# Kernel tuning notes

Measured on AMD Instinct MI355X. Metric: run time of the kernel, lower is better.

The kernel has to match this reference:

```python
import jax, jax.numpy as jnp
import numpy as np

B, S, D, H = 4, 2048, 1024, 16
HD = D // H


def setup_inputs() -> dict:
    key = jax.random.key(0)
    k = jax.random.split(key, 5)
    scale = 0.02
    return {
        "x": jax.random.normal(k[0], (B, S, D), dtype=jnp.float32),
        "Wq": jax.random.normal(k[1], (D, D), dtype=jnp.float32) * scale,
        "Wk": jax.random.normal(k[2], (D, D), dtype=jnp.float32) * scale,
        "Wv": jax.random.normal(k[3], (D, D), dtype=jnp.float32) * scale,
        "Wo": jax.random.normal(k[4], (D, D), dtype=jnp.float32) * scale,
    }


def reference(x, Wq, Wk, Wv, Wo):
    b, s, d_in = x.shape
    h, hd = H, HD
    # projections: [b, s, h, hd] -> [b, h, s, hd]
    q = (x @ Wq).reshape(b, s, h, hd).transpose(0, 2, 1, 3)
    k = (x @ Wk).reshape(b, s, h, hd).transpose(0, 2, 1, 3)
    v = (x @ Wv).reshape(b, s, h, hd).transpose(0, 2, 1, 3)
    # attention scores [b, h, s, s] with causal mask (match original: mask BEFORE scaling)
    scores = jnp.einsum("bhqd,bhkd->bhqk", q, k)
    causal = jnp.triu(jnp.ones((s, s), dtype=bool), k=1)
    scores = jnp.where(causal, -jnp.inf, scores)
    weights = jax.nn.softmax(scores / jnp.sqrt(jnp.float32(hd)), axis=-1)
    ctx = jnp.einsum("bhqk,bhkd->bhqd", weights, v)  # [b, h, s, hd]
    ctx = ctx.transpose(0, 2, 1, 3).reshape(b, s, h * hd)
    return ctx @ Wo
```

## Files before the change

kernel.cpp:

```cpp
#include <hip/hip_runtime.h>

#define SEQ 2048
#define DMODEL 1024
#define NH 16
#define HD 64

typedef unsigned short bf16u;
typedef unsigned short u16x8 __attribute__((ext_vector_type(8)));
typedef unsigned short u16x4 __attribute__((ext_vector_type(4)));
typedef float f32x4 __attribute__((ext_vector_type(4)));

__device__ __forceinline__ unsigned short f2b(float f) {
  __bf16 h = (__bf16)f;
  return __builtin_bit_cast(unsigned short, h);
}

__device__ __forceinline__ f32x4 mfma_bf16(u16x8 a, u16x8 b, f32x4 c) {
  return __builtin_amdgcn_mfma_f32_16x16x32_bf16(a, b, c, 0, 0, 0);
}

__device__ __forceinline__ void load16_lds(const bf16u* g, bf16u* l) {
  __builtin_amdgcn_global_load_lds(
      (const __attribute__((address_space(1))) unsigned int*)(const void*)g,
      (__attribute__((address_space(3))) unsigned int*)(void*)l, 16, 0, 0);
}

__global__ __launch_bounds__(256) void cast_x_kernel(const float4* __restrict__ x,
                                                     u16x4* __restrict__ xb, int n4) {
  int i = blockIdx.x * blockDim.x + threadIdx.x;
  if (i < n4) {
    float4 v = x[i];
    u16x4 o;
    o[0] = f2b(v.x); o[1] = f2b(v.y); o[2] = f2b(v.z); o[3] = f2b(v.w);
    xb[i] = o;
  }
}

__global__ __launch_bounds__(256) void transpose_w_kernel(const float* __restrict__ W0,
                                                          const float* __restrict__ W1,
                                                          const float* __restrict__ W2,
                                                          const float* __restrict__ W3,
                                                          bf16u* __restrict__ T) {
  const float* W = (blockIdx.z == 0) ? W0 : (blockIdx.z == 1) ? W1
                  : (blockIdx.z == 2) ? W2 : W3;
  bf16u* Wt = T + (size_t)blockIdx.z * (DMODEL * DMODEL);
  __shared__ float tile[32][33];
  int n = blockIdx.x * 32 + threadIdx.x;
  int k0 = blockIdx.y * 32;
  for (int i = threadIdx.y; i < 32; i += 8)
    tile[i][threadIdx.x] = W[(size_t)(k0 + i) * DMODEL + n];
  __syncthreads();
  int k = k0 + threadIdx.x;
  int n0 = blockIdx.x * 32;
  for (int i = threadIdx.y; i < 32; i += 8)
    Wt[(size_t)(n0 + i) * DMODEL + k] = f2b(tile[threadIdx.x][i]);
}


__global__ __launch_bounds__(256) void gemm_qkv_kernel(const bf16u* __restrict__ A,
                                                       const bf16u* __restrict__ Wt,
                                                       bf16u* __restrict__ QKV) {
  const bf16u* Bt = Wt + (size_t)blockIdx.z * (DMODEL * DMODEL);
  bf16u* O = QKV + (size_t)blockIdx.z * ((size_t)8192 * DMODEL);
  const bool vmode = (blockIdx.z == 2);

  __shared__ __align__(16) bf16u As[128 * 32];
  __shared__ __align__(16) bf16u Bs[128 * 32];

  const int tid = threadIdx.x;
  const int lane = tid & 63, quad = lane >> 4, l15 = lane & 15;
  const int wave = tid >> 6;
  const int wrow = (wave >> 1) * 64, wcol = (wave & 1) * 64;
  const int mbase = blockIdx.y * 128, nbase = blockIdx.x * 128;

  const int r0 = tid >> 2, s0 = tid & 3;
  const int g0 = s0 ^ (r0 & 3);
  const bf16u* Ag0 = A + (size_t)(mbase + r0) * DMODEL + g0 * 8;
  const bf16u* Bg0 = Bt + (size_t)(nbase + r0) * DMODEL + g0 * 8;
  const bf16u* Ag1 = Ag0 + (size_t)64 * DMODEL;
  const bf16u* Bg1 = Bg0 + (size_t)64 * DMODEL;
  bf16u* Al0 = &As[tid * 8];
  bf16u* Al1 = &As[2048 + tid * 8];
  bf16u* Bl0 = &Bs[tid * 8];
  bf16u* Bl1 = &Bs[2048 + tid * 8];

  const int xq = (quad ^ (l15 & 3)) * 8;

  f32x4 acc[4][4];
#pragma unroll
  for (int i = 0; i < 4; ++i)
#pragma unroll
    for (int j = 0; j < 4; ++j) acc[i][j] = (f32x4){0.f, 0.f, 0.f, 0.f};

  for (int k0 = 0; k0 < DMODEL; k0 += 32) {
    __syncthreads();
    load16_lds(Ag0 + k0, Al0);
    load16_lds(Ag1 + k0, Al1);
    load16_lds(Bg0 + k0, Bl0);
    load16_lds(Bg1 + k0, Bl1);
    __syncthreads();
    u16x8 af[4], bfr[4];
#pragma unroll
    for (int i = 0; i < 4; ++i)
      af[i] = *(const u16x8*)&As[(wrow + i * 16 + l15) * 32 + xq];
#pragma unroll
    for (int j = 0; j < 4; ++j)
      bfr[j] = *(const u16x8*)&Bs[(wcol + j * 16 + l15) * 32 + xq];
#pragma unroll
    for (int i = 0; i < 4; ++i)
#pragma unroll
      for (int j = 0; j < 4; ++j)
        acc[i][j] = mfma_bf16(af[i], bfr[j], acc[i][j]);
  }

#pragma unroll
  for (int i = 0; i < 4; ++i) {
    const int mrow = mbase + wrow + i * 16 + quad * 4;
    const int bb = mrow >> 11, ss = mrow & 2047;
#pragma unroll
    for (int j = 0; j < 4; ++j) {
      const int n = nbase + wcol + j * 16 + l15;
      const int h = n >> 6, hd = n & 63;
      if (vmode) {
        u16x4 pk;
#pragma unroll
        for (int r = 0; r < 4; ++r) pk[r] = f2b(acc[i][j][r]);
        *(u16x4*)&O[(((size_t)(bb * NH + h)) * HD + hd) * SEQ + ss] = pk;
      } else {
#pragma unroll
        for (int r = 0; r < 4; ++r)
          O[(((size_t)(bb * NH + h)) * SEQ + ss + r) * HD + hd] = f2b(acc[i][j][r]);
      }
    }
  }
}

__global__ __launch_bounds__(256) void gemm_out_kernel(const bf16u* __restrict__ A,
                                                       const bf16u* __restrict__ Bt,
                                                       float* __restrict__ Of) {
  __shared__ __align__(16) bf16u As[128 * 32];
  __shared__ __align__(16) bf16u Bs[128 * 32];

  const int tid = threadIdx.x;
  const int lane = tid & 63, quad = lane >> 4, l15 = lane & 15;
  const int wave = tid >> 6;
  const int wrow = (wave >> 1) * 64, wcol = (wave & 1) * 64;
  const int mbase = blockIdx.y * 128, nbase = blockIdx.x * 128;

  const int r0 = tid >> 2, s0 = tid & 3;
  const int g0 = s0 ^ (r0 & 3);
  const bf16u* Ag0 = A + (size_t)(mbase + r0) * DMODEL + g0 * 8;
  const bf16u* Bg0 = Bt + (size_t)(nbase + r0) * DMODEL + g0 * 8;
  const bf16u* Ag1 = Ag0 + (size_t)64 * DMODEL;
  const bf16u* Bg1 = Bg0 + (size_t)64 * DMODEL;
  bf16u* Al0 = &As[tid * 8];
  bf16u* Al1 = &As[2048 + tid * 8];
  bf16u* Bl0 = &Bs[tid * 8];
  bf16u* Bl1 = &Bs[2048 + tid * 8];

  const int xq = (quad ^ (l15 & 3)) * 8;

  f32x4 acc[4][4];
#pragma unroll
  for (int i = 0; i < 4; ++i)
#pragma unroll
    for (int j = 0; j < 4; ++j) acc[i][j] = (f32x4){0.f, 0.f, 0.f, 0.f};

  for (int k0 = 0; k0 < DMODEL; k0 += 32) {
    __syncthreads();
    load16_lds(Ag0 + k0, Al0);
    load16_lds(Ag1 + k0, Al1);
    load16_lds(Bg0 + k0, Bl0);
    load16_lds(Bg1 + k0, Bl1);
    __syncthreads();
    u16x8 af[4], bfr[4];
#pragma unroll
    for (int i = 0; i < 4; ++i)
      af[i] = *(const u16x8*)&As[(wrow + i * 16 + l15) * 32 + xq];
#pragma unroll
    for (int j = 0; j < 4; ++j)
      bfr[j] = *(const u16x8*)&Bs[(wcol + j * 16 + l15) * 32 + xq];
#pragma unroll
    for (int i = 0; i < 4; ++i)
#pragma unroll
      for (int j = 0; j < 4; ++j)
        acc[i][j] = mfma_bf16(af[i], bfr[j], acc[i][j]);
  }

#pragma unroll
  for (int i = 0; i < 4; ++i) {
    const int mrow = mbase + wrow + i * 16 + quad * 4;
#pragma unroll
    for (int j = 0; j < 4; ++j) {
      const int n = nbase + wcol + j * 16 + l15;
#pragma unroll
      for (int r = 0; r < 4; ++r)
        Of[(size_t)(mrow + r) * DMODEL + n] = acc[i][j][r];
    }
  }
}

__global__ __launch_bounds__(256, 2) void attn_kernel(const bf16u* __restrict__ Q,
                                                      const bf16u* __restrict__ K,
                                                      const bf16u* __restrict__ Vt,
                                                      bf16u* __restrict__ ctx) {
  const int bh = blockIdx.y;
  const int b = bh >> 4, h = bh & 15;
  const int bp = blockIdx.x;
  const size_t base = (size_t)bh * SEQ * HD;
  const bf16u* Qb = Q + base;
  const bf16u* Kb = K + base;
  const bf16u* Vb = Vt + base;

  const int tid = threadIdx.x;
  const int wave = tid >> 6, lane = tid & 63, quad = lane >> 4, l15 = lane & 15;

  __shared__ __align__(16) bf16u Ks[64 * 72];
  __shared__ __align__(16) bf16u Vs[64 * 72];
  __shared__ __align__(16) bf16u Ps[4][32 * 68];

  const int srow = tid >> 3;
  const int scol = (tid & 7) * 8;
  const float S = 0.18033688f;

  u16x8 ones;
#pragma unroll
  for (int i = 0; i < 8; ++i) ones[i] = 0x3F80;

#pragma unroll 1
  for (int pi = 0; pi < 2; ++pi) {
    const int qt = pi ? bp : (15 - bp);
    const int qrow0 = qt * 128 + wave * 32;
    const int ntiles = 2 * qt + 2;

    u16x8 aq[2][2];
#pragma unroll
    for (int rt = 0; rt < 2; ++rt)
#pragma unroll
      for (int ch = 0; ch < 2; ++ch)
        aq[rt][ch] = *(const u16x8*)(Qb + (size_t)(qrow0 + rt * 16 + l15) * HD + ch * 32 + quad * 8);

    f32x4 acc[2][4], accl[2];
#pragma unroll
    for (int rt = 0; rt < 2; ++rt) {
#pragma unroll
      for (int nc = 0; nc < 4; ++nc) acc[rt][nc] = (f32x4){0.f, 0.f, 0.f, 0.f};
      accl[rt] = (f32x4){0.f, 0.f, 0.f, 0.f};
    }

    u16x8 kr0 = *(const u16x8*)(Kb + (size_t)srow * HD + scol);
    u16x8 kr1 = *(const u16x8*)(Kb + (size_t)(srow + 32) * HD + scol);
    u16x8 vr0 = *(const u16x8*)(Vb + (size_t)srow * SEQ + scol);
    u16x8 vr1 = *(const u16x8*)(Vb + (size_t)(srow + 32) * SEQ + scol);

#pragma unroll 1
    for (int kt = 0; kt < ntiles; ++kt) {
      const int kbase = kt * 64;
      __syncthreads();
      *(u16x8*)&Ks[srow * 72 + scol] = kr0;
      *(u16x8*)&Ks[(srow + 32) * 72 + scol] = kr1;
      *(u16x8*)&Vs[srow * 72 + scol] = vr0;
      *(u16x8*)&Vs[(srow + 32) * 72 + scol] = vr1;
      __syncthreads();
      if (kt + 1 < ntiles) {
        const int nb = kbase + 64;
        kr0 = *(const u16x8*)(Kb + (size_t)(nb + srow) * HD + scol);
        kr1 = *(const u16x8*)(Kb + (size_t)(nb + srow + 32) * HD + scol);
        vr0 = *(const u16x8*)(Vb + (size_t)srow * SEQ + nb + scol);
        vr1 = *(const u16x8*)(Vb + (size_t)(srow + 32) * SEQ + nb + scol);
      }
      if (kbase > qrow0 + 31) continue;

      f32x4 sc[2][4];
#pragma unroll
      for (int ct = 0; ct < 4; ++ct) {
        u16x8 bk0 = *(const u16x8*)&Ks[(ct * 16 + l15) * 72 + quad * 8];
        u16x8 bk1 = *(const u16x8*)&Ks[(ct * 16 + l15) * 72 + 32 + quad * 8];
#pragma unroll
        for (int rt = 0; rt < 2; ++rt) {
          f32x4 z = {0.f, 0.f, 0.f, 0.f};
          z = mfma_bf16(aq[rt][0], bk0, z);
          z = mfma_bf16(aq[rt][1], bk1, z);
          sc[rt][ct] = z;
        }
      }

      const bool needmask = (kbase + 63 > qrow0);
#pragma unroll
      for (int rt = 0; rt < 2; ++rt) {
#pragma unroll
        for (int r = 0; r < 4; ++r) {
          const int row = qrow0 + rt * 16 + quad * 4 + r;
          float e0 = exp2f(sc[rt][0][r] * S);
          float e1 = exp2f(sc[rt][1][r] * S);
          float e2 = exp2f(sc[rt][2][r] * S);
          float e3 = exp2f(sc[rt][3][r] * S);
          if (needmask) {
            if (kbase + l15 > row) e0 = 0.f;
            if (kbase + 16 + l15 > row) e1 = 0.f;
            if (kbase + 32 + l15 > row) e2 = 0.f;
            if (kbase + 48 + l15 > row) e3 = 0.f;
          }
          const int prow = (rt * 16 + quad * 4 + r) * 68;
          Ps[wave][prow + l15] = f2b(e0);
          Ps[wave][prow + 16 + l15] = f2b(e1);
          Ps[wave][prow + 32 + l15] = f2b(e2);
          Ps[wave][prow + 48 + l15] = f2b(e3);
        }
      }

      u16x8 pa[2][2];
#pragma unroll
      for (int rt = 0; rt < 2; ++rt)
#pragma unroll
        for (int ch = 0; ch < 2; ++ch)
          pa[rt][ch] = *(const u16x8*)&Ps[wave][(rt * 16 + l15) * 68 + ch * 32 + quad * 8];

#pragma unroll
      for (int nc = 0; nc < 4; ++nc) {
        u16x8 bv0 = *(const u16x8*)&Vs[(nc * 16 + l15) * 72 + quad * 8];
        u16x8 bv1 = *(const u16x8*)&Vs[(nc * 16 + l15) * 72 + 32 + quad * 8];
#pragma unroll
        for (int rt = 0; rt < 2; ++rt) {
          acc[rt][nc] = mfma_bf16(pa[rt][0], bv0, acc[rt][nc]);
          acc[rt][nc] = mfma_bf16(pa[rt][1], bv1, acc[rt][nc]);
        }
      }
#pragma unroll
      for (int rt = 0; rt < 2; ++rt) {
        accl[rt] = mfma_bf16(pa[rt][0], ones, accl[rt]);
        accl[rt] = mfma_bf16(pa[rt][1], ones, accl[rt]);
      }
    }

#pragma unroll
    for (int rt = 0; rt < 2; ++rt) {
#pragma unroll
      for (int r = 0; r < 4; ++r) {
        const float inv = 1.0f / accl[rt][r];
        const int row = qrow0 + rt * 16 + quad * 4 + r;
        const size_t o = ((size_t)b * SEQ + row) * DMODEL + h * HD;
#pragma unroll
        for (int nc = 0; nc < 4; ++nc)
          ctx[o + nc * 16 + l15] = f2b(acc[rt][nc][r] * inv);
      }
    }
  }
}

extern "C" void kernel_launch(void* const* d_in, const int* in_sizes, int n_in,
                              void* d_out, int out_size, void* d_ws, size_t ws_size,
                              hipStream_t stream) {
  const float* x  = (const float*)d_in[0];
  const float* Wq = (const float*)d_in[1];
  const float* Wk = (const float*)d_in[2];
  const float* Wv = (const float*)d_in[3];
  const float* Wo = (const float*)d_in[4];
  float* out = (float*)d_out;

  char* ws = (char*)d_ws;
  const size_t MK = (size_t)8192 * DMODEL;
  const size_t WW = (size_t)DMODEL * DMODEL;
  bf16u* xb  = (bf16u*)ws;
  bf16u* Wt  = (bf16u*)(ws + MK * 2);
  bf16u* QKV = (bf16u*)(ws + MK * 2 + 4 * WW * 2);
  bf16u* Cx  = (bf16u*)(ws + MK * 2 + 4 * WW * 2 + 3 * MK * 2);

  const int n4 = (int)(MK / 4);
  cast_x_kernel<<<dim3(n4 / 256), 256, 0, stream>>>((const float4*)x, (u16x4*)xb, n4);
  transpose_w_kernel<<<dim3(32, 32, 4), dim3(32, 8), 0, stream>>>(Wq, Wk, Wv, Wo, Wt);
  gemm_qkv_kernel<<<dim3(8, 64, 3), 256, 0, stream>>>(xb, Wt, QKV);
  attn_kernel<<<dim3(8, 64), 256, 0, stream>>>(QKV, QKV + MK, QKV + 2 * MK, Cx);
  gemm_out_kernel<<<dim3(8, 64), 256, 0, stream>>>(Cx, Wt + 3 * WW, out);
}
```

Measured before the change: 280.8 us.

## Split attention to one query tile per block, fold softmax scale into Q

```diff
diff --git a/kernel.cpp b/kernel.cpp
--- a/kernel.cpp
+++ b/kernel.cpp
@@ -63,6 +63,7 @@
   const bf16u* Bt = Wt + (size_t)blockIdx.z * (DMODEL * DMODEL);
   bf16u* O = QKV + (size_t)blockIdx.z * ((size_t)8192 * DMODEL);
   const bool vmode = (blockIdx.z == 2);
+  const float smul = (blockIdx.z == 0) ? 0.18033688f : 1.0f;
 
   __shared__ __align__(16) bf16u As[128 * 32];
   __shared__ __align__(16) bf16u Bs[128 * 32];
@@ -129,66 +130,63 @@
       } else {
 #pragma unroll
         for (int r = 0; r < 4; ++r)
-          O[(((size_t)(bb * NH + h)) * SEQ + ss + r) * HD + hd] = f2b(acc[i][j][r]);
+          O[(((size_t)(bb * NH + h)) * SEQ + ss + r) * HD + hd] = f2b(acc[i][j][r] * smul);
       }
     }
   }
 }
 
-__global__ __launch_bounds__(256) void gemm_out_kernel(const bf16u* __restrict__ A,
-                                                       const bf16u* __restrict__ Bt,
-                                                       float* __restrict__ Of) {
-  __shared__ __align__(16) bf16u As[128 * 32];
+__global__ __launch_bounds__(256, 2) void gemm_out_kernel(const bf16u* __restrict__ A,
+                                                          const bf16u* __restrict__ Bt,
+                                                          float* __restrict__ Of) {
+  __shared__ __align__(16) bf16u As[64 * 32];
   __shared__ __align__(16) bf16u Bs[128 * 32];
 
   const int tid = threadIdx.x;
   const int lane = tid & 63, quad = lane >> 4, l15 = lane & 15;
   const int wave = tid >> 6;
-  const int wrow = (wave >> 1) * 64, wcol = (wave & 1) * 64;
-  const int mbase = blockIdx.y * 128, nbase = blockIdx.x * 128;
+  const int wrow = (wave >> 1) * 32, wcol = (wave & 1) * 64;
+  const int mbase = blockIdx.y * 64, nbase = blockIdx.x * 128;
 
   const int r0 = tid >> 2, s0 = tid & 3;
   const int g0 = s0 ^ (r0 & 3);
   const bf16u* Ag0 = A + (size_t)(mbase + r0) * DMODEL + g0 * 8;
   const bf16u* Bg0 = Bt + (size_t)(nbase + r0) * DMODEL + g0 * 8;
-  const bf16u* Ag1 = Ag0 + (size_t)64 * DMODEL;
   const bf16u* Bg1 = Bg0 + (size_t)64 * DMODEL;
   bf16u* Al0 = &As[tid * 8];
-  bf16u* Al1 = &As[2048 + tid * 8];
   bf16u* Bl0 = &Bs[tid * 8];
   bf16u* Bl1 = &Bs[2048 + tid * 8];
 
   const int xq = (quad ^ (l15 & 3)) * 8;
 
-  f32x4 acc[4][4];
-#pragma unroll
-  for (int i = 0; i < 4; ++i)
+  f32x4 acc[2][4];
+#pragma unroll
+  for (int i = 0; i < 2; ++i)
 #pragma unroll
     for (int j = 0; j < 4; ++j) acc[i][j] = (f32x4){0.f, 0.f, 0.f, 0.f};
 
   for (int k0 = 0; k0 < DMODEL; k0 += 32) {
     __syncthreads();
     load16_lds(Ag0 + k0, Al0);
-    load16_lds(Ag1 + k0, Al1);
     load16_lds(Bg0 + k0, Bl0);
     load16_lds(Bg1 + k0, Bl1);
     __syncthreads();
-    u16x8 af[4], bfr[4];
-#pragma unroll
-    for (int i = 0; i < 4; ++i)
+    u16x8 af[2], bfr[4];
+#pragma unroll
+    for (int i = 0; i < 2; ++i)
       af[i] = *(const u16x8*)&As[(wrow + i * 16 + l15) * 32 + xq];
 #pragma unroll
     for (int j = 0; j < 4; ++j)
       bfr[j] = *(const u16x8*)&Bs[(wcol + j * 16 + l15) * 32 + xq];
 #pragma unroll
-    for (int i = 0; i < 4; ++i)
+    for (int i = 0; i < 2; ++i)
 #pragma unroll
       for (int j = 0; j < 4; ++j)
         acc[i][j] = mfma_bf16(af[i], bfr[j], acc[i][j]);
   }
 
 #pragma unroll
-  for (int i = 0; i < 4; ++i) {
+  for (int i = 0; i < 2; ++i) {
     const int mrow = mbase + wrow + i * 16 + quad * 4;
 #pragma unroll
     for (int j = 0; j < 4; ++j) {
@@ -200,13 +198,13 @@
   }
 }
 
-__global__ __launch_bounds__(256, 2) void attn_kernel(const bf16u* __restrict__ Q,
+__global__ __launch_bounds__(256, 4) void attn_kernel(const bf16u* __restrict__ Q,
                                                       const bf16u* __restrict__ K,
                                                       const bf16u* __restrict__ Vt,
                                                       bf16u* __restrict__ ctx) {
   const int bh = blockIdx.y;
   const int b = bh >> 4, h = bh & 15;
-  const int bp = blockIdx.x;
+  const int qt = 15 - blockIdx.x;
   const size_t base = (size_t)bh * SEQ * HD;
   const bf16u* Qb = Q + base;
   const bf16u* Kb = K + base;
@@ -214,136 +212,126 @@
 
   const int tid = threadIdx.x;
   const int wave = tid >> 6, lane = tid & 63, quad = lane >> 4, l15 = lane & 15;
+  const int qrow0 = qt * 128 + wave * 32;
+  const int ntiles = 2 * qt + 2;
 
   __shared__ __align__(16) bf16u Ks[64 * 72];
   __shared__ __align__(16) bf16u Vs[64 * 72];
-  __shared__ __align__(16) bf16u Ps[4][32 * 68];
+  __shared__ __align__(16) bf16u Ps[4][16 * 68];
 
   const int srow = tid >> 3;
   const int scol = (tid & 7) * 8;
-  const float S = 0.18033688f;
 
   u16x8 ones;
 #pragma unroll
   for (int i = 0; i < 8; ++i) ones[i] = 0x3F80;
 
+  u16x8 aq[2][2];
+#pragma unroll
+  for (int rt = 0; rt < 2; ++rt)
+#pragma unroll
+    for (int ch = 0; ch < 2; ++ch)
+      aq[rt][ch] = *(const u16x8*)(Qb + (size_t)(qrow0 + rt * 16 + l15) * HD + ch * 32 + quad * 8);
+
+  f32x4 acc[2][4], accl[2];
+#pragma unroll
+  for (int rt = 0; rt < 2; ++rt) {
+#pragma unroll
+    for (int nc = 0; nc < 4; ++nc) acc[rt][nc] = (f32x4){0.f, 0.f, 0.f, 0.f};
+    accl[rt] = (f32x4){0.f, 0.f, 0.f, 0.f};
+  }
+
+  u16x8 kr0 = *(const u16x8*)(Kb + (size_t)srow * HD + scol);
+  u16x8 kr1 = *(const u16x8*)(Kb + (size_t)(srow + 32) * HD + scol);
+  u16x8 vr0 = *(const u16x8*)(Vb + (size_t)srow * SEQ + scol);
+  u16x8 vr1 = *(const u16x8*)(Vb + (size_t)(srow + 32) * SEQ + scol);
+
 #pragma unroll 1
-  for (int pi = 0; pi < 2; ++pi) {
-    const int qt = pi ? bp : (15 - bp);
-    const int qrow0 = qt * 128 + wave * 32;
-    const int ntiles = 2 * qt + 2;
-
-    u16x8 aq[2][2];
-#pragma unroll
-    for (int rt = 0; rt < 2; ++rt)
-#pragma unroll
-      for (int ch = 0; ch < 2; ++ch)
-        aq[rt][ch] = *(const u16x8*)(Qb + (size_t)(qrow0 + rt * 16 + l15) * HD + ch * 32 + quad * 8);
-
-    f32x4 acc[2][4], accl[2];
+  for (int kt = 0; kt < ntiles; ++kt) {
+    const int kbase = kt * 64;
+    __syncthreads();
+    *(u16x8*)&Ks[srow * 72 + scol] = kr0;
+    *(u16x8*)&Ks[(srow + 32) * 72 + scol] = kr1;
+    *(u16x8*)&Vs[srow * 72 + scol] = vr0;
+    *(u16x8*)&Vs[(srow + 32) * 72 + scol] = vr1;
+    __syncthreads();
+    if (kt + 1 < ntiles) {
+      const int nb = kbase + 64;
+      kr0 = *(const u16x8*)(Kb + (size_t)(nb + srow) * HD + scol);
+      kr1 = *(const u16x8*)(Kb + (size_t)(nb + srow + 32) * HD + scol);
+      vr0 = *(const u16x8*)(Vb + (size_t)srow * SEQ + nb + scol);
+      vr1 = *(const u16x8*)(Vb + (size_t)(srow + 32) * SEQ + nb + scol);
+    }
+    if (kbase > qrow0 + 31) continue;
+
+    f32x4 sc[2][4];
+#pragma unroll
+    for (int ct = 0; ct < 4; ++ct) {
+      u16x8 bk0 = *(const u16x8*)&Ks[(ct * 16 + l15) * 72 + quad * 8];
+      u16x8 bk1 = *(const u16x8*)&Ks[(ct * 16 + l15) * 72 + 32 + quad * 8];
+#pragma unroll
+      for (int rt = 0; rt < 2; ++rt) {
+        f32x4 z = {0.f, 0.f, 0.f, 0.f};
+        z = mfma_bf16(aq[rt][0], bk0, z);
+        z = mfma_bf16(aq[rt][1], bk1, z);
+        sc[rt][ct] = z;
+      }
+    }
+
+    const bool needmask = (kbase + 63 > qrow0);
+    u16x8 pa[2][2];
 #pragma unroll
     for (int rt = 0; rt < 2; ++rt) {
 #pragma unroll
-      for (int nc = 0; nc < 4; ++nc) acc[rt][nc] = (f32x4){0.f, 0.f, 0.f, 0.f};
-      accl[rt] = (f32x4){0.f, 0.f, 0.f, 0.f};
-    }
-
-    u16x8 kr0 = *(const u16x8*)(Kb + (size_t)srow * HD + scol);
-    u16x8 kr1 = *(const u16x8*)(Kb + (size_t)(srow + 32) * HD + scol);
-    u16x8 vr0 = *(const u16x8*)(Vb + (size_t)srow * SEQ + scol);
-    u16x8 vr1 = *(const u16x8*)(Vb + (size_t)(srow + 32) * SEQ + scol);
-
-#pragma unroll 1
-    for (int kt = 0; kt < ntiles; ++kt) {
-      const int kbase = kt * 64;
-      __syncthreads();
-      *(u16x8*)&Ks[srow * 72 + scol] = kr0;
-      *(u16x8*)&Ks[(srow + 32) * 72 + scol] = kr1;
-      *(u16x8*)&Vs[srow * 72 + scol] = vr0;
-      *(u16x8*)&Vs[(srow + 32) * 72 + scol] = vr1;
-      __syncthreads();
-      if (kt + 1 < ntiles) {
-        const int nb = kbase + 64;
-        kr0 = *(const u16x8*)(Kb + (size_t)(nb + srow) * HD + scol);
-        kr1 = *(const u16x8*)(Kb + (size_t)(nb + srow + 32) * HD + scol);
-        vr0 = *(const u16x8*)(Vb + (size_t)srow * SEQ + nb + scol);
-        vr1 = *(const u16x8*)(Vb + (size_t)(srow + 32) * SEQ + nb + scol);
+      for (int r = 0; r < 4; ++r) {
+        const int row = qrow0 + rt * 16 + quad * 4 + r;
+        float e0 = exp2f(sc[rt][0][r]);
+        float e1 = exp2f(sc[rt][1][r]);
+        float e2 = exp2f(sc[rt][2][r]);
+        float e3 = exp2f(sc[rt][3][r]);
+        if (needmask) {
+          if (kbase + l15 > row) e0 = 0.f;
+          if (kbase + 16 + l15 > row) e1 = 0.f;
+          if (kbase + 32 + l15 > row) e2 = 0.f;
+          if (kbase + 48 + l15 > row) e3 = 0.f;
+        }
+        const int prow = (quad * 4 + r) * 68;
+        Ps[wave][prow + l15] = f2b(e0);
+        Ps[wave][prow + 16 + l15] = f2b(e1);
+        Ps[wave][prow + 32 + l15] = f2b(e2);
+        Ps[wave][prow + 48 + l15] = f2b(e3);
       }
-      if (kbase > qrow0 + 31) continue;
-
-      f32x4 sc[2][4];
-#pragma unroll
-      for (int ct = 0; ct < 4; ++ct) {
-        u16x8 bk0 = *(const u16x8*)&Ks[(ct * 16 + l15) * 72 + quad * 8];
-        u16x8 bk1 = *(const u16x8*)&Ks[(ct * 16 + l15) * 72 + 32 + quad * 8];
-#pragma unroll
-        for (int rt = 0; rt < 2; ++rt) {
-          f32x4 z = {0.f, 0.f, 0.f, 0.f};
-          z = mfma_bf16(aq[rt][0], bk0, z);
-          z = mfma_bf16(aq[rt][1], bk1, z);
-          sc[rt][ct] = z;
-        }
+      pa[rt][0] = *(const u16x8*)&Ps[wave][l15 * 68 + quad * 8];
+      pa[rt][1] = *(const u16x8*)&Ps[wave][l15 * 68 + 32 + quad * 8];
+    }
+
+#pragma unroll
+    for (int nc = 0; nc < 4; ++nc) {
+      u16x8 bv0 = *(const u16x8*)&Vs[(nc * 16 + l15) * 72 + quad * 8];
+      u16x8 bv1 = *(const u16x8*)&Vs[(nc * 16 + l15) * 72 + 32 + quad * 8];
+#pragma unroll
+      for (int rt = 0; rt < 2; ++rt) {
+        acc[rt][nc] = mfma_bf16(pa[rt][0], bv0, acc[rt][nc]);
+        acc[rt][nc] = mfma_bf16(pa[rt][1], bv1, acc[rt][nc]);
       }
-
-      const bool needmask = (kbase + 63 > qrow0);
-#pragma unroll
-      for (int rt = 0; rt < 2; ++rt) {
-#pragma unroll
-        for (int r = 0; r < 4; ++r) {
-          const int row = qrow0 + rt * 16 + quad * 4 + r;
-          float e0 = exp2f(sc[rt][0][r] * S);
-          float e1 = exp2f(sc[rt][1][r] * S);
-          float e2 = exp2f(sc[rt][2][r] * S);
-          float e3 = exp2f(sc[rt][3][r] * S);
-          if (needmask) {
-            if (kbase + l15 > row) e0 = 0.f;
-            if (kbase + 16 + l15 > row) e1 = 0.f;
-            if (kbase + 32 + l15 > row) e2 = 0.f;
-            if (kbase + 48 + l15 > row) e3 = 0.f;
-          }
-          const int prow = (rt * 16 + quad * 4 + r) * 68;
-          Ps[wave][prow + l15] = f2b(e0);
-          Ps[wave][prow + 16 + l15] = f2b(e1);
-          Ps[wave][prow + 32 + l15] = f2b(e2);
-          Ps[wave][prow + 48 + l15] = f2b(e3);
-        }
-      }
-
-      u16x8 pa[2][2];
-#pragma unroll
-      for (int rt = 0; rt < 2; ++rt)
-#pragma unroll
-        for (int ch = 0; ch < 2; ++ch)
-          pa[rt][ch] = *(const u16x8*)&Ps[wave][(rt * 16 + l15) * 68 + ch * 32 + quad * 8];
-
-#pragma unroll
-      for (int nc = 0; nc < 4; ++nc) {
-        u16x8 bv0 = *(const u16x8*)&Vs[(nc * 16 + l15) * 72 + quad * 8];
-        u16x8 bv1 = *(const u16x8*)&Vs[(nc * 16 + l15) * 72 + 32 + quad * 8];
-#pragma unroll
-        for (int rt = 0; rt < 2; ++rt) {
-          acc[rt][nc] = mfma_bf16(pa[rt][0], bv0, acc[rt][nc]);
-          acc[rt][nc] = mfma_bf16(pa[rt][1], bv1, acc[rt][nc]);
-        }
-      }
-#pragma unroll
-      for (int rt = 0; rt < 2; ++rt) {
-        accl[rt] = mfma_bf16(pa[rt][0], ones, accl[rt]);
-        accl[rt] = mfma_bf16(pa[rt][1], ones, accl[rt]);
-      }
-    }
-
+    }
 #pragma unroll
     for (int rt = 0; rt < 2; ++rt) {
-#pragma unroll
-      for (int r = 0; r < 4; ++r) {
-        const float inv = 1.0f / accl[rt][r];
-        const int row = qrow0 + rt * 16 + quad * 4 + r;
-        const size_t o = ((size_t)b * SEQ + row) * DMODEL + h * HD;
-#pragma unroll
-        for (int nc = 0; nc < 4; ++nc)
-          ctx[o + nc * 16 + l15] = f2b(acc[rt][nc][r] * inv);
-      }
+      accl[rt] = mfma_bf16(pa[rt][0], ones, accl[rt]);
+      accl[rt] = mfma_bf16(pa[rt][1], ones, accl[rt]);
+    }
+  }
+
+#pragma unroll
+  for (int rt = 0; rt < 2; ++rt) {
+#pragma unroll
+    for (int r = 0; r < 4; ++r) {
+      const float inv = 1.0f / accl[rt][r];
+      const int row = qrow0 + rt * 16 + quad * 4 + r;
+      const size_t o = ((size_t)b * SEQ + row) * DMODEL + h * HD;
+#pragma unroll
+      for (int nc = 0; nc < 4; ++nc)
+        ctx[o + nc * 16 + l15] = f2b(acc[rt][nc][r] * inv);
     }
   }
 }
@@ -370,6 +358,6 @@
   cast_x_kernel<<<dim3(n4 / 256), 256, 0, stream>>>((const float4*)x, (u16x4*)xb, n4);
   transpose_w_kernel<<<dim3(32, 32, 4), dim3(32, 8), 0, stream>>>(Wq, Wk, Wv, Wo, Wt);
   gemm_qkv_kernel<<<dim3(8, 64, 3), 256, 0, stream>>>(xb, Wt, QKV);
-  attn_kernel<<<dim3(8, 64), 256, 0, stream>>>(QKV, QKV + MK, QKV + 2 * MK, Cx);
-  gemm_out_kernel<<<dim3(8, 64), 256, 0, stream>>>(Cx, Wt + 3 * WW, out);
-}
+  attn_kernel<<<dim3(16, 64), 256, 0, stream>>>(QKV, QKV + MK, QKV + 2 * MK, Cx);
+  gemm_out_kernel<<<dim3(8, 128), 256, 0, stream>>>(Cx, Wt + 3 * WW, out);
+}
```

After: 321.8 us. 1.15x slower.

## Double-buffer LDS tiles in GEMMs and fold softmax scale into Q projection

Applied to the files above, without the earlier changes.

```diff
diff --git a/kernel.cpp b/kernel.cpp
--- a/kernel.cpp
+++ b/kernel.cpp
@@ -24,6 +24,8 @@
       (const __attribute__((address_space(1))) unsigned int*)(const void*)g,
       (__attribute__((address_space(3))) unsigned int*)(void*)l, 16, 0, 0);
 }
+
+#define WAITCNT_VM(n) __builtin_amdgcn_s_waitcnt(0x0F70 | (n))
 
 __global__ __launch_bounds__(256) void cast_x_kernel(const float4* __restrict__ x,
                                                      u16x4* __restrict__ xb, int n4) {
@@ -63,9 +65,10 @@
   const bf16u* Bt = Wt + (size_t)blockIdx.z * (DMODEL * DMODEL);
   bf16u* O = QKV + (size_t)blockIdx.z * ((size_t)8192 * DMODEL);
   const bool vmode = (blockIdx.z == 2);
-
-  __shared__ __align__(16) bf16u As[128 * 32];
-  __shared__ __align__(16) bf16u Bs[128 * 32];
+  const float smul = (blockIdx.z == 0) ? 0.18033688f : 1.0f;
+
+  __shared__ __align__(16) bf16u As[2][128 * 32];
+  __shared__ __align__(16) bf16u Bs[2][128 * 32];
 
   const int tid = threadIdx.x;
   const int lane = tid & 63, quad = lane >> 4, l15 = lane & 15;
@@ -79,10 +82,6 @@
   const bf16u* Bg0 = Bt + (size_t)(nbase + r0) * DMODEL + g0 * 8;
   const bf16u* Ag1 = Ag0 + (size_t)64 * DMODEL;
   const bf16u* Bg1 = Bg0 + (size_t)64 * DMODEL;
-  bf16u* Al0 = &As[tid * 8];
-  bf16u* Al1 = &As[2048 + tid * 8];
-  bf16u* Bl0 = &Bs[tid * 8];
-  bf16u* Bl1 = &Bs[2048 + tid * 8];
 
   const int xq = (quad ^ (l15 & 3)) * 8;
 
@@ -92,25 +91,38 @@
 #pragma unroll
     for (int j = 0; j < 4; ++j) acc[i][j] = (f32x4){0.f, 0.f, 0.f, 0.f};
 
-  for (int k0 = 0; k0 < DMODEL; k0 += 32) {
-    __syncthreads();
-    load16_lds(Ag0 + k0, Al0);
-    load16_lds(Ag1 + k0, Al1);
-    load16_lds(Bg0 + k0, Bl0);
-    load16_lds(Bg1 + k0, Bl1);
-    __syncthreads();
+  load16_lds(Ag0, &As[0][tid * 8]);
+  load16_lds(Ag1, &As[0][2048 + tid * 8]);
+  load16_lds(Bg0, &Bs[0][tid * 8]);
+  load16_lds(Bg1, &Bs[0][2048 + tid * 8]);
+
+#pragma unroll 1
+  for (int it = 0; it < 32; ++it) {
+    const int cur = it & 1, nxt = cur ^ 1;
+    if (it + 1 < 32) {
+      const int kn = (it + 1) * 32;
+      load16_lds(Ag0 + kn, &As[nxt][tid * 8]);
+      load16_lds(Ag1 + kn, &As[nxt][2048 + tid * 8]);
+      load16_lds(Bg0 + kn, &Bs[nxt][tid * 8]);
+      load16_lds(Bg1 + kn, &Bs[nxt][2048 + tid * 8]);
+      WAITCNT_VM(4);
+    } else {
+      WAITCNT_VM(0);
+    }
+    __builtin_amdgcn_s_barrier();
     u16x8 af[4], bfr[4];
 #pragma unroll
     for (int i = 0; i < 4; ++i)
-      af[i] = *(const u16x8*)&As[(wrow + i * 16 + l15) * 32 + xq];
+      af[i] = *(const u16x8*)&As[cur][(wrow + i * 16 + l15) * 32 + xq];
 #pragma unroll
     for (int j = 0; j < 4; ++j)
-      bfr[j] = *(const u16x8*)&Bs[(wcol + j * 16 + l15) * 32 + xq];
+      bfr[j] = *(const u16x8*)&Bs[cur][(wcol + j * 16 + l15) * 32 + xq];
 #pragma unroll
     for (int i = 0; i < 4; ++i)
 #pragma unroll
       for (int j = 0; j < 4; ++j)
         acc[i][j] = mfma_bf16(af[i], bfr[j], acc[i][j]);
+    __builtin_amdgcn_s_barrier();
   }
 
 #pragma unroll
@@ -129,7 +141,7 @@
       } else {
 #pragma unroll
         for (int r = 0; r < 4; ++r)
-          O[(((size_t)(bb * NH + h)) * SEQ + ss + r) * HD + hd] = f2b(acc[i][j][r]);
+          O[(((size_t)(bb * NH + h)) * SEQ + ss + r) * HD + hd] = f2b(acc[i][j][r] * smul);
       }
     }
   }
@@ -138,8 +150,8 @@
 __global__ __launch_bounds__(256) void gemm_out_kernel(const bf16u* __restrict__ A,
                                                        const bf16u* __restrict__ Bt,
                                                        float* __restrict__ Of) {
-  __shared__ __align__(16) bf16u As[128 * 32];
-  __shared__ __align__(16) bf16u Bs[128 * 32];
+  __shared__ __align__(16) bf16u As[2][128 * 32];
+  __shared__ __align__(16) bf16u Bs[2][128 * 32];
 
   const int tid = threadIdx.x;
   const int lane = tid & 63, quad = lane >> 4, l15 = lane & 15;
@@ -153,10 +165,6 @@
   const bf16u* Bg0 = Bt + (size_t)(nbase + r0) * DMODEL + g0 * 8;
   const bf16u* Ag1 = Ag0 + (size_t)64 * DMODEL;
   const bf16u* Bg1 = Bg0 + (size_t)64 * DMODEL;
-  bf16u* Al0 = &As[tid * 8];
-  bf16u* Al1 = &As[2048 + tid * 8];
-  bf16u* Bl0 = &Bs[tid * 8];
-  bf16u* Bl1 = &Bs[2048 + tid * 8];
 
   const int xq = (quad ^ (l15 & 3)) * 8;
 
@@ -166,25 +174,38 @@
 #pragma unroll
     for (int j = 0; j < 4; ++j) acc[i][j] = (f32x4){0.f, 0.f, 0.f, 0.f};
 
-  for (int k0 = 0; k0 < DMODEL; k0 += 32) {
-    __syncthreads();
-    load16_lds(Ag0 + k0, Al0);
-    load16_lds(Ag1 + k0, Al1);
-    load16_lds(Bg0 + k0, Bl0);
-    load16_lds(Bg1 + k0, Bl1);
-    __syncthreads();
+  load16_lds(Ag0, &As[0][tid * 8]);
+  load16_lds(Ag1, &As[0][2048 + tid * 8]);
+  load16_lds(Bg0, &Bs[0][tid * 8]);
+  load16_lds(Bg1, &Bs[0][2048 + tid * 8]);
+
+#pragma unroll 1
+  for (int it = 0; it < 32; ++it) {
+    const int cur = it & 1, nxt = cur ^ 1;
+    if (it + 1 < 32) {
+      const int kn = (it + 1) * 32;
+      load16_lds(Ag0 + kn, &As[nxt][tid * 8]);
+      load16_lds(Ag1 + kn, &As[nxt][2048 + tid * 8]);
+      load16_lds(Bg0 + kn, &Bs[nxt][tid * 8]);
+      load16_lds(Bg1 + kn, &Bs[nxt][2048 + tid * 8]);
+      WAITCNT_VM(4);
+    } else {
+      WAITCNT_VM(0);
+    }
+    __builtin_amdgcn_s_barrier();
     u16x8 af[4], bfr[4];
 #pragma unroll
     for (int i = 0; i < 4; ++i)
-      af[i] = *(const u16x8*)&As[(wrow + i * 16 + l15) * 32 + xq];
+      af[i] = *(const u16x8*)&As[cur][(wrow + i * 16 + l15) * 32 + xq];
 #pragma unroll
     for (int j = 0; j < 4; ++j)
-      bfr[j] = *(const u16x8*)&Bs[(wcol + j * 16 + l15) * 32 + xq];
+      bfr[j] = *(const u16x8*)&Bs[cur][(wcol + j * 16 + l15) * 32 + xq];
 #pragma unroll
     for (int i = 0; i < 4; ++i)
 #pragma unroll
       for (int j = 0; j < 4; ++j)
         acc[i][j] = mfma_bf16(af[i], bfr[j], acc[i][j]);
+    __builtin_amdgcn_s_barrier();
   }
 
 #pragma unroll
@@ -221,7 +242,6 @@
 
   const int srow = tid >> 3;
   const int scol = (tid & 7) * 8;
-  const float S = 0.18033688f;
 
   u16x8 ones;
 #pragma unroll
@@ -291,10 +311,10 @@
 #pragma unroll
         for (int r = 0; r < 4; ++r) {
           const int row = qrow0 + rt * 16 + quad * 4 + r;
-          float e0 = exp2f(sc[rt][0][r] * S);
-          float e1 = exp2f(sc[rt][1][r] * S);
-          float e2 = exp2f(sc[rt][2][r] * S);
-          float e3 = exp2f(sc[rt][3][r] * S);
+          float e0 = exp2f(sc[rt][0][r]);
+          float e1 = exp2f(sc[rt][1][r]);
+          float e2 = exp2f(sc[rt][2][r]);
+          float e3 = exp2f(sc[rt][3][r]);
           if (needmask) {
             if (kbase + l15 > row) e0 = 0.f;
             if (kbase + 16 + l15 > row) e1 = 0.f;
```

After: 274.0 us. 2.4% less time.
